# Kernel optimization log

Measured on AMD Instinct MI355X. Metric: run time of the kernel, lower is better.

Reference implementation:

```python
import jax, jax.numpy as jnp
import numpy as np

G = 131072            # number of graphs
NPG = 38              # nodes per graph (from reshape to (*, 38))
N = G * NPG           # total nodes
E = 10 * N            # total edges (avg degree 10)


def leaky_relu(x):
    return jnp.where(x >= 0, x, 0.01 * x)


def setup_inputs() -> dict:
    key = jax.random.key(0)
    ks = jax.random.split(key, 13)
    s = 0.1
    return {
        "x": jax.random.normal(ks[0], (N, 1), jnp.float32),
        "edge_index": jax.random.randint(ks[1], (2, E), 0, N, dtype=jnp.int64)
            if jax.config.read("jax_enable_x64") else jax.random.randint(ks[1], (2, E), 0, N, dtype=jnp.int32),
        "edge_attr": jax.random.normal(ks[2], (E, 1), jnp.float32),
        # NNConv(1,1, Linear(1,1)) params
        "w_edge": jax.random.normal(ks[3], (1, 1), jnp.float32) * s,  # edge MLP weight
        "b_edge": jax.random.normal(ks[4], (1,), jnp.float32) * s,   # edge MLP bias
        "w_root": jax.random.normal(ks[5], (1, 1), jnp.float32) * s, # NNConv root weight
        "b_conv": jax.random.normal(ks[6], (1,), jnp.float32) * s,   # NNConv bias
        # head MLP: 38 -> 4 -> 4 -> 12 (stored as (in, out))
        "W1": jax.random.normal(ks[7], (38, 4), jnp.float32) * s,
        "b1": jax.random.normal(ks[8], (4,), jnp.float32) * s,
        "W2": jax.random.normal(ks[9], (4, 4), jnp.float32) * s,
        "b2": jax.random.normal(ks[10], (4,), jnp.float32) * s,
        "W3": jax.random.normal(ks[11], (4, 12), jnp.float32) * s,
        "b3": jax.random.normal(ks[12], (12,), jnp.float32) * s,
    }


def reference(x, edge_index, edge_attr, w_edge, b_edge, w_root, b_conv,
              W1, b1, W2, b2, W3, b3):
    src, dst = edge_index[0], edge_index[1]
    # per-edge 1x1 transform produced by edge MLP: theta_e = Linear(edge_attr)
    theta = edge_attr @ w_edge + b_edge            # [E, 1]
    # message = x_src * theta (in=out=1 so the matmul is a scalar product)
    msg = x[src] * theta                           # [E, 1] gather + multiply
    agg = jax.ops.segment_sum(msg, dst, num_segments=N)  # scatter-add to targets
    nodes = agg + x @ w_root + b_conv              # [N, 1] add aggr + root + bias
    # dense head over per-graph node vectors (dropout is identity at eval)
    h = nodes.reshape(G, NPG)                      # [G, 38]
    h = leaky_relu(h @ W1 + b1)                    # [G, 4]
    h = leaky_relu(h @ W2 + b2)                    # [G, 4]
    h = leaky_relu(h @ W3 + b3)                    # [G, 12]
    return jax.nn.softmax(h, axis=-1)
```

## Files before the change

kernel.cpp:

```cpp
#include <hip/hip_runtime.h>
#include <hip/hip_fp16.h>

#define NPG 38
#define HEAD_BLK 256
#define SHIFT 13
#define SLICE (1 << SHIFT)
#define DBMAX 640
#define NSB 8
#define NB1 1024
#define P1_THR 512
#define CH 8192
#define P2_THR 512
#define BB_THR 1024
#define BB_PH 1024

typedef int      v4i __attribute__((ext_vector_type(4)));
typedef float    v4f __attribute__((ext_vector_type(4)));
typedef unsigned v2u __attribute__((ext_vector_type(2)));

static inline __device__ unsigned short f2h(float f) {
    return __half_as_ushort(__float2half(f));
}
static inline __device__ float h2f(unsigned short b) {
    return __half2float(__ushort_as_half(b));
}

__global__ __launch_bounds__(P1_THR) void k_p1a(
    const int* __restrict__ src, int nquads, int qpb, int sbsz,
    int* __restrict__ histM8)
{
    __shared__ int h8[NSB];
    const int tid = threadIdx.x;
    if (tid < NSB) h8[tid] = 0;
    __syncthreads();
    const int blk = blockIdx.x;
    const int q0 = blk * qpb;
    const int q1 = min(q0 + qpb, nquads);
    const v4i* s4 = (const v4i*)src;
    for (int q = q0 + tid; q < q1; q += P1_THR) {
        v4i s = __builtin_nontemporal_load(s4 + q);
        atomicAdd(&h8[s.x / sbsz], 1);
        atomicAdd(&h8[s.y / sbsz], 1);
        atomicAdd(&h8[s.z / sbsz], 1);
        atomicAdd(&h8[s.w / sbsz], 1);
    }
    __syncthreads();
    if (tid < NSB) histM8[tid * NB1 + blk] = h8[tid];
}

__global__ __launch_bounds__(512) void k_scanM(
    int* __restrict__ histM8, int* __restrict__ sseg)
{
    __shared__ int stot[NSB];
    __shared__ int sbase[NSB + 1];
    const int tid = threadIdx.x;
    const int wid = tid >> 6, lane = tid & 63;

    const int base = wid * NB1 + lane * (NB1 / 64);
    int vals[NB1 / 64];
    int s = 0;
    #pragma unroll
    for (int k = 0; k < NB1 / 64; ++k) { vals[k] = s; s += histM8[base + k]; }
    int excl = s;
    #pragma unroll
    for (int d = 1; d < 64; d <<= 1) {
        int t = __shfl_up(excl, d, 64);
        if (lane >= d) excl += t;
    }
    excl -= s;
    if (lane == 63) stot[wid] = excl + s;
    __syncthreads();
    if (tid == 0) {
        int run = 0;
        for (int i = 0; i < NSB; ++i) { sbase[i] = run; run += stot[i]; }
        sbase[NSB] = run;
    }
    __syncthreads();
    const int b0 = sbase[wid] + excl;
    #pragma unroll
    for (int k = 0; k < NB1 / 64; ++k) histM8[base + k] = vals[k] + b0;
    if (tid < NSB + 1) sseg[tid] = sbase[tid];
}

__global__ __launch_bounds__(P1_THR) void k_p1b(
    const int* __restrict__ src, const int* __restrict__ dst,
    const float* __restrict__ ea,
    const float* __restrict__ w_edge, const float* __restrict__ b_edge,
    int nquads, int qpb, int sbsz,
    const int* __restrict__ histM8,
    v2u* __restrict__ recs)
{
    __shared__ int cur8[NSB];
    const int blk = blockIdx.x;
    if (threadIdx.x < NSB) cur8[threadIdx.x] = histM8[threadIdx.x * NB1 + blk];
    __syncthreads();
    const int q0 = blk * qpb;
    const int q1 = min(q0 + qpb, nquads);
    const float we = w_edge[0], be = b_edge[0];
    const v4i* s4 = (const v4i*)src;
    const v4i* d4 = (const v4i*)dst;
    const v4f* e4 = (const v4f*)ea;
    for (int q = q0 + threadIdx.x; q < q1; q += P1_THR) {
        v4i s = __builtin_nontemporal_load(s4 + q);
        v4i d = __builtin_nontemporal_load(d4 + q);
        v4f e = __builtin_nontemporal_load(e4 + q);
        #pragma unroll
        for (int k = 0; k < 4; ++k) {
            int sv = (k == 0) ? s.x : (k == 1) ? s.y : (k == 2) ? s.z : s.w;
            int dv = (k == 0) ? d.x : (k == 1) ? d.y : (k == 2) ? d.z : d.w;
            float ev = (k == 0) ? e.x : (k == 1) ? e.y : (k == 2) ? e.z : e.w;
            int sb = sv / sbsz;
            int sl = sv - sb * sbsz;
            unsigned short tb = f2h(fmaf(ev, we, be));
            int p = atomicAdd(&cur8[sb], 1);
            v2u r;
            r.x = ((unsigned)(sl & 0xFFFF) << 16) | (unsigned)tb;
            r.y = (unsigned)dv | ((unsigned)(sl >> 16) << 23);
            recs[p] = r;
        }
    }
}

__global__ __launch_bounds__(P2_THR) void k_p2(
    const v2u* __restrict__ recs, const float* __restrict__ x,
    const int* __restrict__ sseg, int sbsz, int DB, int NCH, int bpx, int E,
    unsigned short* __restrict__ ofsT, unsigned* __restrict__ pairs)
{
    __shared__ __align__(16) unsigned pairbuf[CH];
    __shared__ int hD[DBMAX];
    __shared__ int lofs[DBMAX];
    __shared__ int lcur[DBMAX];
    __shared__ int sS[NSB + 1];

    const int jraw = blockIdx.x;
    const int j = (jraw & 7) * bpx + (jraw >> 3);
    if (j >= NCH) return;
    const int start = j * CH;
    const int n = min(CH, E - start);
    const int tid = threadIdx.x;
    const int wid = tid >> 6, lane = tid & 63;

    if (tid < NSB + 1) sS[tid] = sseg[tid];
    for (int i = tid; i < DBMAX; i += P2_THR) hD[i] = 0;
    __syncthreads();

    #pragma unroll
    for (int half = 0; half < CH / (8 * P2_THR); ++half) {
        unsigned bk[8];
        #pragma unroll
        for (int k = 0; k < 8; ++k) {
            int idx = tid + (half * 8 + k) * P2_THR;
            bk[k] = (idx < n) ? ((recs[start + idx].y & 0x7FFFFFu) >> SHIFT)
                              : 0xFFFFu;
        }
        #pragma unroll
        for (int k = 0; k < 8; ++k)
            if (bk[k] != 0xFFFFu) atomicAdd(&hD[bk[k]], 1);
    }
    __syncthreads();

    if (wid == 0) {
        const int base = lane * (DBMAX / 64);
        int vals[DBMAX / 64];
        int s = 0;
        #pragma unroll
        for (int k = 0; k < DBMAX / 64; ++k) { vals[k] = s; s += hD[base + k]; }
        int excl = s;
        #pragma unroll
        for (int d = 1; d < 64; d <<= 1) {
            int t = __shfl_up(excl, d, 64);
            if (lane >= d) excl += t;
        }
        excl -= s;
        #pragma unroll
        for (int k = 0; k < DBMAX / 64; ++k) lofs[base + k] = vals[k] + excl;
    }
    __syncthreads();

    const size_t tbase = (size_t)j * (DBMAX + 1);
    for (int b = tid; b < DB; b += P2_THR) {
        lcur[b] = lofs[b];
        ofsT[tbase + b] = (unsigned short)lofs[b];
    }
    if (tid == 0) ofsT[tbase + DB] = (unsigned short)n;
    __syncthreads();

    #pragma unroll
    for (int half = 0; half < CH / (8 * P2_THR); ++half) {
        v2u r[8];
        #pragma unroll
        for (int k = 0; k < 8; ++k) {
            int idx = tid + (half * 8 + k) * P2_THR;
            if (idx < n) r[k] = recs[start + idx];
            else { r[k].x = 0u; r[k].y = 0u; }
        }
        float xv[8];
        #pragma unroll
        for (int k = 0; k < 8; ++k) {
            int idx = tid + (half * 8 + k) * P2_THR;
            int gp = start + min(idx, n - 1);
            int sbr = 0;
            #pragma unroll
            for (int s = 1; s < NSB; ++s) sbr += (gp >= sS[s]);
            int sl = (int)(r[k].x >> 16) | (int)((r[k].y >> 23) << 16);
            xv[k] = x[(size_t)sbr * sbsz + sl];
        }
        #pragma unroll
        for (int k = 0; k < 8; ++k) {
            int idx = tid + (half * 8 + k) * P2_THR;
            if (idx < n) {
                unsigned d = r[k].y & 0x7FFFFFu;
                float m = xv[k] * h2f((unsigned short)(r[k].x & 0xFFFFu));
                int li = atomicAdd(&lcur[d >> SHIFT], 1);
                pairbuf[li] = ((d & (SLICE - 1)) << 16) | (unsigned)f2h(m);
            }
        }
    }
    __syncthreads();

    const size_t pbase = (size_t)j * CH;
    uint4* out4 = reinterpret_cast<uint4*>(pairs + pbase);
    const uint4* pb4 = reinterpret_cast<const uint4*>(pairbuf);
    #pragma unroll
    for (int i = 0; i < CH / 4 / P2_THR; ++i)
        out4[tid + i * P2_THR] = pb4[tid + i * P2_THR];
}

__global__ __launch_bounds__(BB_THR) void k_binB(
    const unsigned* __restrict__ pairs,
    const unsigned short* __restrict__ ofsT,
    int NCH, int DB,
    const float* __restrict__ x,
    const float* __restrict__ w_root, const float* __restrict__ b_conv,
    float* __restrict__ nodes, int N)
{
    __shared__ float slice[SLICE];
    __shared__ unsigned short so0[BB_PH];
    __shared__ int spre[BB_PH];
    __shared__ int sTot;
    const int b = blockIdx.x;
    const int tid = threadIdx.x;
    const int wid = tid >> 6, lane = tid & 63;

    for (int i = tid; i < SLICE; i += BB_THR) slice[i] = 0.0f;
    __syncthreads();

    for (int ch0 = 0; ch0 < NCH; ch0 += BB_PH) {
        const int nc = min(BB_PH, NCH - ch0);
        for (int c = tid; c < nc; c += BB_THR) {
            const size_t tb = (size_t)(ch0 + c) * (DBMAX + 1);
            int o0 = ofsT[tb + b];
            int o1 = ofsT[tb + b + 1];
            so0[c] = (unsigned short)o0;
            spre[c] = o1 - o0;
        }
        __syncthreads();
        if (wid == 0) {
            const int base = lane * (BB_PH / 64);
            int vals[BB_PH / 64];
            int s = 0;
            #pragma unroll
            for (int k = 0; k < BB_PH / 64; ++k) {
                int idx = base + k;
                int t = (idx < nc) ? spre[idx] : 0;
                vals[k] = s; s += t;
            }
            int excl = s;
            #pragma unroll
            for (int d = 1; d < 64; d <<= 1) {
                int t = __shfl_up(excl, d, 64);
                if (lane >= d) excl += t;
            }
            excl -= s;
            #pragma unroll
            for (int k = 0; k < BB_PH / 64; ++k) {
                int idx = base + k;
                if (idx < nc) spre[idx] = vals[k] + excl;
            }
            if (lane == 63) sTot = excl + s;
        }
        __syncthreads();
        const int total = sTot;
        for (int i = tid; i < total; i += BB_THR) {
            int lo = 0, hi = nc - 1;
            while (lo < hi) {
                int mid = (lo + hi + 1) >> 1;
                if (spre[mid] <= i) lo = mid; else hi = mid - 1;
            }
            int off = i - spre[lo];
            unsigned p = pairs[(size_t)(ch0 + lo) * CH + so0[lo] + off];
            atomicAdd(&slice[p >> 16], h2f((unsigned short)(p & 0xFFFFu)));
        }
        __syncthreads();
    }

    const float wr = w_root[0], bc = b_conv[0];
    const int gbase = b << SHIFT;
    for (int i = tid; i < SLICE; i += BB_THR) {
        int gi = gbase + i;
        if (gi < N) nodes[gi] = slice[i] + fmaf(__builtin_nontemporal_load(x + gi), wr, bc);
    }
}

__global__ __launch_bounds__(512) void k_count_mid(
    const int* __restrict__ dst, int nquads, int qpb, int DB,
    int* __restrict__ gcntD)
{
    __shared__ int hD[DBMAX];
    for (int i = threadIdx.x; i < DB; i += 512) hD[i] = 0;
    __syncthreads();
    const int q0 = blockIdx.x * qpb;
    const int q1 = min(q0 + qpb, nquads);
    const v4i* d4 = (const v4i*)dst;
    for (int q = q0 + threadIdx.x; q < q1; q += 512) {
        v4i d = __builtin_nontemporal_load(d4 + q);
        atomicAdd(&hD[d.x >> SHIFT], 1);
        atomicAdd(&hD[d.y >> SHIFT], 1);
        atomicAdd(&hD[d.z >> SHIFT], 1);
        atomicAdd(&hD[d.w >> SHIFT], 1);
    }
    __syncthreads();
    for (int i = threadIdx.x; i < DB; i += 512)
        if (hD[i]) atomicAdd(&gcntD[i], hD[i]);
}

__global__ void k_scanD(const int* __restrict__ gcntD, int DB,
                        int* __restrict__ bbaseD, int* __restrict__ gcurD)
{
    if (threadIdx.x == 0 && blockIdx.x == 0) {
        int run = 0;
        for (int i = 0; i < DB; ++i) { bbaseD[i] = run; gcurD[i] = run; run += gcntD[i]; }
        bbaseD[DB] = run;
    }
}

__global__ __launch_bounds__(512) void k_binA_resv(
    const float* __restrict__ x,
    const int* __restrict__ src, const int* __restrict__ dst,
    const float* __restrict__ ea,
    const float* __restrict__ w_edge, const float* __restrict__ b_edge,
    int nquads, int qpb, int DB,
    int* __restrict__ gcurD, unsigned* __restrict__ pairs)
{
    __shared__ int hD[DBMAX];
    __shared__ int cur[DBMAX];
    const int q0 = blockIdx.x * qpb;
    const int q1 = min(q0 + qpb, nquads);
    for (int i = threadIdx.x; i < DB; i += 512) hD[i] = 0;
    __syncthreads();
    const v4i* s4 = (const v4i*)src;
    const v4i* d4 = (const v4i*)dst;
    const v4f* e4 = (const v4f*)ea;
    for (int q = q0 + threadIdx.x; q < q1; q += 512) {
        v4i d = d4[q];
        atomicAdd(&hD[d.x >> SHIFT], 1);
        atomicAdd(&hD[d.y >> SHIFT], 1);
        atomicAdd(&hD[d.z >> SHIFT], 1);
        atomicAdd(&hD[d.w >> SHIFT], 1);
    }
    __syncthreads();
    for (int i = threadIdx.x; i < DB; i += 512) {
        int cnt = hD[i];
        cur[i] = cnt ? atomicAdd(&gcurD[i], cnt) : 0;
    }
    __syncthreads();
    const float we = w_edge[0], be = b_edge[0];
    for (int q = q0 + threadIdx.x; q < q1; q += 512) {
        v4i s = __builtin_nontemporal_load(s4 + q);
        v4i d = d4[q];
        v4f e = __builtin_nontemporal_load(e4 + q);
        #pragma unroll
        for (int k = 0; k < 4; ++k) {
            int sv = (k == 0) ? s.x : (k == 1) ? s.y : (k == 2) ? s.z : s.w;
            unsigned dv = (unsigned)((k == 0) ? d.x : (k == 1) ? d.y : (k == 2) ? d.z : d.w);
            float ev = (k == 0) ? e.x : (k == 1) ? e.y : (k == 2) ? e.z : e.w;
            float m = x[sv] * fmaf(ev, we, be);
            int p = atomicAdd(&cur[dv >> SHIFT], 1);
            pairs[p] = ((dv & (SLICE - 1)) << 16) | (unsigned)f2h(m);
        }
    }
}

__global__ __launch_bounds__(1024) void k_binB_lin(
    const unsigned* __restrict__ pairs,
    const int* __restrict__ bbaseD,
    const float* __restrict__ x,
    const float* __restrict__ w_root, const float* __restrict__ b_conv,
    float* __restrict__ nodes, int N)
{
    __shared__ float slice[SLICE];
    const int b = blockIdx.x;
    for (int i = threadIdx.x; i < SLICE; i += 1024) slice[i] = 0.0f;
    __syncthreads();
    const int p0 = bbaseD[b];
    const int p1 = bbaseD[b + 1];
    for (int i = p0 + threadIdx.x; i < p1; i += 1024) {
        unsigned p = __builtin_nontemporal_load(pairs + i);
        atomicAdd(&slice[p >> 16], h2f((unsigned short)(p & 0xFFFFu)));
    }
    __syncthreads();
    const float wr = w_root[0], bc = b_conv[0];
    const int gbase = b << SHIFT;
    for (int i = threadIdx.x; i < SLICE; i += 1024) {
        int gi = gbase + i;
        if (gi < N) nodes[gi] = slice[i] + fmaf(__builtin_nontemporal_load(x + gi), wr, bc);
    }
}

__global__ __launch_bounds__(256) void edge_kernel_atomic(
    const float* __restrict__ x,
    const int*   __restrict__ src, const int* __restrict__ dst,
    const float* __restrict__ ea,
    const float* __restrict__ w_edge, const float* __restrict__ b_edge,
    float* __restrict__ agg, int E)
{
    const float we = w_edge[0], be = b_edge[0];
    int tid = blockIdx.x * blockDim.x + threadIdx.x;
    int stride = gridDim.x * blockDim.x;
    for (int i = tid; i < E; i += stride)
        atomicAdd(&agg[dst[i]], x[src[i]] * fmaf(ea[i], we, be));
}

__global__ __launch_bounds__(256) void finalize_nodes(
    const float* __restrict__ x, const float* __restrict__ agg,
    const float* __restrict__ w_root, const float* __restrict__ b_conv,
    float* __restrict__ nodes, int N)
{
    const float wr = w_root[0], bc = b_conv[0];
    int i = blockIdx.x * blockDim.x + threadIdx.x;
    int stride = gridDim.x * blockDim.x;
    for (; i < N; i += stride) nodes[i] = agg[i] + fmaf(x[i], wr, bc);
}

__global__ __launch_bounds__(HEAD_BLK) void head_kernel(
    const float* __restrict__ nodes,
    const float* __restrict__ W1, const float* __restrict__ b1,
    const float* __restrict__ W2, const float* __restrict__ b2,
    const float* __restrict__ W3, const float* __restrict__ b3,
    float* __restrict__ out, int G)
{
    __shared__ float s_nodes[HEAD_BLK * NPG];
    __shared__ float s_W1[NPG * 4];
    __shared__ float s_W2[4 * 4];
    __shared__ float s_W3[4 * 12];
    __shared__ float s_b1[4];
    __shared__ float s_b2[4];
    __shared__ float s_b3[12];

    const int tid = threadIdx.x;
    if (tid < NPG * 4) s_W1[tid] = W1[tid];
    if (tid >= 160 && tid < 176) s_W2[tid - 160] = W2[tid - 160];
    if (tid >= 176 && tid < 224) s_W3[tid - 176] = W3[tid - 176];
    if (tid >= 224 && tid < 228) s_b1[tid - 224] = b1[tid - 224];
    if (tid >= 228 && tid < 232) s_b2[tid - 228] = b2[tid - 228];
    if (tid >= 232 && tid < 244) s_b3[tid - 232] = b3[tid - 232];

    const int g0 = blockIdx.x * HEAD_BLK;
    const size_t ebase = (size_t)g0 * NPG;
    const int nelem = HEAD_BLK * NPG;
    const int avail = min(nelem, (G - g0) * NPG);
    for (int i = tid; i < avail; i += HEAD_BLK) s_nodes[i] = nodes[ebase + i];
    __syncthreads();

    const int g = g0 + tid;
    if (g >= G) return;
    const float* nd = &s_nodes[tid * NPG];

    float h1[4];
    #pragma unroll
    for (int k = 0; k < 4; ++k) h1[k] = s_b1[k];
    #pragma unroll
    for (int j = 0; j < NPG; ++j) {
        const float nj = nd[j];
        #pragma unroll
        for (int k = 0; k < 4; ++k) h1[k] = fmaf(nj, s_W1[j * 4 + k], h1[k]);
    }
    #pragma unroll
    for (int k = 0; k < 4; ++k) h1[k] = h1[k] >= 0.0f ? h1[k] : 0.01f * h1[k];

    float h2[4];
    #pragma unroll
    for (int k = 0; k < 4; ++k) {
        float a = s_b2[k];
        #pragma unroll
        for (int j = 0; j < 4; ++j) a = fmaf(h1[j], s_W2[j * 4 + k], a);
        h2[k] = a >= 0.0f ? a : 0.01f * a;
    }

    float h3[12];
    #pragma unroll
    for (int k = 0; k < 12; ++k) {
        float a = s_b3[k];
        #pragma unroll
        for (int j = 0; j < 4; ++j) a = fmaf(h2[j], s_W3[j * 12 + k], a);
        h3[k] = a >= 0.0f ? a : 0.01f * a;
    }

    float m = h3[0];
    #pragma unroll
    for (int k = 1; k < 12; ++k) m = fmaxf(m, h3[k]);
    float sum = 0.0f;
    #pragma unroll
    for (int k = 0; k < 12; ++k) { h3[k] = expf(h3[k] - m); sum += h3[k]; }
    const float inv = 1.0f / sum;

    float4* o = reinterpret_cast<float4*>(out + (size_t)g * 12);
    o[0] = make_float4(h3[0] * inv, h3[1] * inv, h3[2]  * inv, h3[3]  * inv);
    o[1] = make_float4(h3[4] * inv, h3[5] * inv, h3[6]  * inv, h3[7]  * inv);
    o[2] = make_float4(h3[8] * inv, h3[9] * inv, h3[10] * inv, h3[11] * inv);
}

extern "C" void kernel_launch(void* const* d_in, const int* in_sizes, int n_in,
                              void* d_out, int out_size, void* d_ws, size_t ws_size,
                              hipStream_t stream)
{
    const float* x      = (const float*)d_in[0];
    const int*   eidx   = (const int*)  d_in[1];
    const float* ea     = (const float*)d_in[2];
    const float* w_edge = (const float*)d_in[3];
    const float* b_edge = (const float*)d_in[4];
    const float* w_root = (const float*)d_in[5];
    const float* b_conv = (const float*)d_in[6];
    const float* W1 = (const float*)d_in[7];
    const float* b1 = (const float*)d_in[8];
    const float* W2 = (const float*)d_in[9];
    const float* b2 = (const float*)d_in[10];
    const float* W3 = (const float*)d_in[11];
    const float* b3 = (const float*)d_in[12];
    float* out = (float*)d_out;

    const int N = in_sizes[0];
    const int E = in_sizes[2];
    const int G = N / NPG;
    const int* src = eidx;
    const int* dst = eidx + E;
    const int nquads = E / 4;
    const int DB = (N + SLICE - 1) >> SHIFT;

    const int hblocks = (G + HEAD_BLK - 1) / HEAD_BLK;
    char* ws = (char*)d_ws;

    const bool quadok = (E % 4) == 0 && DB <= DBMAX && DB >= 1;
    const int  sbsz   = (N % NSB == 0) ? (N / NSB) : 0;

    const int NCH = (E + CH - 1) / CH;
    const int bpx = (NCH + 7) / 8;

    const size_t META_INTS = (size_t)NSB * NB1 + (NSB + 1) + DBMAX + DBMAX + (DBMAX + 1);

    size_t off_pairs = (size_t)E * 8;
    size_t sz_pairs  = (size_t)NCH * CH * 4;
    size_t off_ofsT  = off_pairs + sz_pairs;
    size_t sz_ofsT   = ((size_t)NCH * (DBMAX + 1) * 2 + 15) & ~(size_t)15;
    size_t off_nodes = off_ofsT + sz_ofsT;
    size_t off_meta  = off_nodes + (size_t)N * 4;
    size_t need_v5   = off_meta + META_INTS * 4;

    size_t off_nodes_mid = (size_t)E * 4;
    size_t off_meta_mid  = off_nodes_mid + (size_t)N * 4;
    size_t need_mid      = off_meta_mid + META_INTS * 4;

    if (quadok && sbsz > 0 && need_v5 <= ws_size) {
        v2u*            recs  = (v2u*)ws;
        unsigned*       pairs = (unsigned*)(ws + off_pairs);
        unsigned short* ofsT  = (unsigned short*)(ws + off_ofsT);
        float*          nodes = (float*)(ws + off_nodes);
        int*            meta  = (int*)(ws + off_meta);
        int* histM8 = meta;
        int* sseg   = meta + NSB * NB1;

        const int qpb = (nquads + NB1 - 1) / NB1;
        k_p1a<<<NB1, P1_THR, 0, stream>>>(src, nquads, qpb, sbsz, histM8);
        k_scanM<<<1, 512, 0, stream>>>(histM8, sseg);
        k_p1b<<<NB1, P1_THR, 0, stream>>>(src, dst, ea, w_edge, b_edge,
                                          nquads, qpb, sbsz, histM8, recs);
        k_p2<<<8 * bpx, P2_THR, 0, stream>>>(recs, x, sseg, sbsz, DB, NCH, bpx,
                                             E, ofsT, pairs);
        k_binB<<<DB, BB_THR, 0, stream>>>(pairs, ofsT, NCH, DB, x,
                                          w_root, b_conv, nodes, N);
        head_kernel<<<hblocks, HEAD_BLK, 0, stream>>>(nodes, W1, b1, W2, b2,
                                                      W3, b3, out, G);
    } else if (quadok && need_mid <= ws_size) {
        unsigned* pairs = (unsigned*)ws;
        float*    nodes = (float*)(ws + off_nodes_mid);
        int*      meta  = (int*)(ws + off_meta_mid);
        int* gcntD  = meta + NSB * NB1 + (NSB + 1);
        int* gcurD  = gcntD + DBMAX;
        int* bbaseD = gcurD + DBMAX;

        hipMemsetAsync(gcntD, 0, DBMAX * sizeof(int), stream);
        const int NBm = 2048;
        const int qpbm = (nquads + NBm - 1) / NBm;
        k_count_mid<<<NBm, 512, 0, stream>>>(dst, nquads, qpbm, DB, gcntD);
        k_scanD<<<1, 64, 0, stream>>>(gcntD, DB, bbaseD, gcurD);
        k_binA_resv<<<NBm, 512, 0, stream>>>(x, src, dst, ea, w_edge, b_edge,
                                             nquads, qpbm, DB, gcurD, pairs);
        k_binB_lin<<<DB, 1024, 0, stream>>>(pairs, bbaseD, x, w_root, b_conv,
                                            nodes, N);
        head_kernel<<<hblocks, HEAD_BLK, 0, stream>>>(nodes, W1, b1, W2, b2,
                                                      W3, b3, out, G);
    } else {
        float* agg   = (float*)d_ws;
        float* nodes = agg + N;
        hipMemsetAsync(agg, 0, (size_t)N * sizeof(float), stream);
        edge_kernel_atomic<<<2048, 256, 0, stream>>>(x, src, dst, ea, w_edge,
                                                     b_edge, agg, E);
        finalize_nodes<<<2048, 256, 0, stream>>>(x, agg, w_root, b_conv, nodes, N);
        head_kernel<<<hblocks, HEAD_BLK, 0, stream>>>(nodes, W1, b1, W2, b2,
                                                      W3, b3, out, G);
    }
}
```

Before: 1.099 ms.

## Replace prefix-scan plus binary search in binB with per-wave chunk-segment processing

The bin-B scatter kernel previously ran a single-wave prefix scan over chunk segment lengths, then had every thread binary-search the prefix array to find its pair. Now each wave takes 8 chunk segments at a time and lanes index directly into each segment, batching 8 loads before issuing the LDS atomics. This removes the serial scan, one barrier and the per-element binary search. In exchange, lanes sit idle whenever a segment is shorter than 64 entries, which is likely given roughly 8192/640 pairs per chunk-bin.

```diff
diff --git a/kernel.cpp b/kernel.cpp
--- a/kernel.cpp
+++ b/kernel.cpp
@@ -12,6 +12,7 @@
 #define CH 8192
 #define P2_THR 512
 #define BB_THR 1024
+#define BB_NW (BB_THR / 64)
 #define BB_PH 1024
 
 typedef int      v4i __attribute__((ext_vector_type(4)));
@@ -236,8 +237,7 @@
 {
     __shared__ float slice[SLICE];
     __shared__ unsigned short so0[BB_PH];
-    __shared__ int spre[BB_PH];
-    __shared__ int sTot;
+    __shared__ unsigned short sln[BB_PH];
     const int b = blockIdx.x;
     const int tid = threadIdx.x;
     const int wid = tid >> 6, lane = tid & 63;
@@ -252,44 +252,38 @@
             int o0 = ofsT[tb + b];
             int o1 = ofsT[tb + b + 1];
             so0[c] = (unsigned short)o0;
-            spre[c] = o1 - o0;
+            sln[c] = (unsigned short)(o1 - o0);
         }
         __syncthreads();
-        if (wid == 0) {
-            const int base = lane * (BB_PH / 64);
-            int vals[BB_PH / 64];
-            int s = 0;
+        for (int c0 = wid * 8; c0 < nc; c0 += BB_NW * 8) {
+            int o0r[8], lnr[8];
             #pragma unroll
-            for (int k = 0; k < BB_PH / 64; ++k) {
-                int idx = base + k;
-                int t = (idx < nc) ? spre[idx] : 0;
-                vals[k] = s; s += t;
+            for (int k = 0; k < 8; ++k) {
+                int c = c0 + k;
+                bool v = c < nc;
+                o0r[k] = v ? (int)so0[c] : 0;
+                lnr[k] = v ? (int)sln[c] : 0;
             }
-            int excl = s;
+            unsigned pr[8];
             #pragma unroll
-            for (int d = 1; d < 64; d <<= 1) {
-                int t = __shfl_up(excl, d, 64);
-                if (lane >= d) excl += t;
+            for (int k = 0; k < 8; ++k) {
+                if (lane < lnr[k])
+                    pr[k] = pairs[(size_t)(ch0 + c0 + k) * CH + o0r[k] + lane];
             }
-            excl -= s;
             #pragma unroll
-            for (int k = 0; k < BB_PH / 64; ++k) {
-                int idx = base + k;
-                if (idx < nc) spre[idx] = vals[k] + excl;
+            for (int k = 0; k < 8; ++k) {
+                if (lane < lnr[k])
+                    atomicAdd(&slice[pr[k] >> 16],
+                              h2f((unsigned short)(pr[k] & 0xFFFFu)));
             }
-            if (lane == 63) sTot = excl + s;
-        }
-        __syncthreads();
-        const int total = sTot;
-        for (int i = tid; i < total; i += BB_THR) {
-            int lo = 0, hi = nc - 1;
-            while (lo < hi) {
-                int mid = (lo + hi + 1) >> 1;
-                if (spre[mid] <= i) lo = mid; else hi = mid - 1;
+            #pragma unroll
+            for (int k = 0; k < 8; ++k) {
+                for (int j2 = lane + 64; j2 < lnr[k]; j2 += 64) {
+                    unsigned p = pairs[(size_t)(ch0 + c0 + k) * CH + o0r[k] + j2];
+                    atomicAdd(&slice[p >> 16],
+                              h2f((unsigned short)(p & 0xFFFFu)));
+                }
             }
-            int off = i - spre[lo];
-            unsigned p = pairs[(size_t)(ch0 + lo) * CH + so0[lo] + off];
-            atomicAdd(&slice[p >> 16], h2f((unsigned short)(p & 0xFFFFu)));
         }
         __syncthreads();
     }
```

Result: no change. 1.108 ms (+0.8%).

## Compact per-chunk bin segments into contiguous buffer before slice accumulation

Applied to the files above, without the earlier changes.

Replaces the binB kernel, which scanned chunk offsets per phase and binary-searched to gather scattered pair segments, with a three-step compaction. The new steps compute per-group bin counts, prefix-sum them, and copy each bin's segments into a contiguous pairs2 buffer (aliasing the recs region). The linear binB kernel then streams contiguous pairs into shared-memory atomics. This removes the per-element binary search and strided gathers, at the cost of an extra full read/write pass over pairs and three more launches, one of them a single-block serial scan.

```diff
diff --git a/kernel.cpp b/kernel.cpp
--- a/kernel.cpp
+++ b/kernel.cpp
@@ -11,8 +11,7 @@
 #define P1_THR 512
 #define CH 8192
 #define P2_THR 512
-#define BB_THR 1024
-#define BB_PH 1024
+#define CGS 64
 
 typedef int      v4i __attribute__((ext_vector_type(4)));
 typedef float    v4f __attribute__((ext_vector_type(4)));
@@ -226,77 +225,143 @@
         out4[tid + i * P2_THR] = pb4[tid + i * P2_THR];
 }
 
-__global__ __launch_bounds__(BB_THR) void k_binB(
+__global__ __launch_bounds__(1024) void k_sum1(
+    const unsigned short* __restrict__ ofsT,
+    int NCH, int DB, int* __restrict__ partial)
+{
+    const int cg = blockIdx.x;
+    const int j0 = cg * CGS;
+    const int jn = min(CGS, NCH - j0);
+    const int b = threadIdx.x;
+    if (b >= DB) return;
+    int acc = 0;
+    for (int k = 0; k < jn; ++k) {
+        size_t tb = (size_t)(j0 + k) * (DBMAX + 1);
+        acc += (int)ofsT[tb + b + 1] - (int)ofsT[tb + b];
+    }
+    partial[(size_t)cg * DB + b] = acc;
+}
+
+__global__ __launch_bounds__(1024) void k_sum2(
+    const int* __restrict__ partial, int ncg, int DB,
+    int* __restrict__ groupbase, int* __restrict__ bbaseD)
+{
+    __shared__ int btot[DBMAX];
+    __shared__ int bofs[DBMAX];
+    const int tid = threadIdx.x;
+    const int wid = tid >> 6, lane = tid & 63;
+    for (int i = tid; i < DBMAX; i += 1024) btot[i] = 0;
+    __syncthreads();
+    if (tid < DB) {
+        int run = 0;
+        for (int cg = 0; cg < ncg; ++cg) {
+            int t = partial[(size_t)cg * DB + tid];
+            groupbase[(size_t)cg * DB + tid] = run;
+            run += t;
+        }
+        btot[tid] = run;
+    }
+    __syncthreads();
+    if (wid == 0) {
+        const int base = lane * (DBMAX / 64);
+        int vals[DBMAX / 64];
+        int s = 0;
+        #pragma unroll
+        for (int k = 0; k < DBMAX / 64; ++k) { vals[k] = s; s += btot[base + k]; }
+        int excl = s;
+        #pragma unroll
+        for (int d = 1; d < 64; d <<= 1) {
+            int t = __shfl_up(excl, d, 64);
+            if (lane >= d) excl += t;
+        }
+        excl -= s;
+        #pragma unroll
+        for (int k = 0; k < DBMAX / 64; ++k) bofs[base + k] = vals[k] + excl;
+    }
+    __syncthreads();
+    if (tid < DB) {
+        int bb = bofs[tid];
+        bbaseD[tid] = bb;
+        for (int cg = 0; cg < ncg; ++cg)
+            groupbase[(size_t)cg * DB + tid] += bb;
+    }
+    if (tid == DB - 1) bbaseD[DB] = bofs[tid] + btot[tid];
+}
+
+__global__ __launch_bounds__(1024) void k_p2b(
     const unsigned* __restrict__ pairs,
     const unsigned short* __restrict__ ofsT,
-    int NCH, int DB,
+    const int* __restrict__ groupbase,
+    int NCH, int DB, int ncg,
+    unsigned* __restrict__ pairs2)
+{
+    const int g  = blockIdx.x & 7;
+    const int cg = blockIdx.x >> 3;
+    if (cg >= ncg) return;
+    const int bpb = (DB + 7) >> 3;
+    const int b0 = g * bpb;
+    const int b1 = min(b0 + bpb, DB);
+    const int j0 = cg * CGS;
+    const int jn = min(CGS, NCH - j0);
+    const int wid = threadIdx.x >> 6, lane = threadIdx.x & 63;
+
+    for (int b = b0 + wid; b < b1; b += 16) {
+        int cur = groupbase[(size_t)cg * DB + b];
+        int o0 = 0, len = 0;
+        if (lane < jn) {
+            size_t tb = (size_t)(j0 + lane) * (DBMAX + 1);
+            o0 = ofsT[tb + b];
+            len = (int)ofsT[tb + b + 1] - o0;
+        }
+        for (int k = 0; k < jn; k += 8) {
+            int ro[8], rl[8], rc[8];
+            int c = cur;
+            #pragma unroll
+            for (int u = 0; u < 8; ++u) {
+                int l = __shfl(len, k + u, 64);
+                ro[u] = __shfl(o0, k + u, 64);
+                rl[u] = (k + u < jn) ? l : 0;
+                rc[u] = c; c += rl[u];
+            }
+            unsigned v[8];
+            #pragma unroll
+            for (int u = 0; u < 8; ++u)
+                if (lane < rl[u])
+                    v[u] = pairs[(size_t)(j0 + k + u) * CH + ro[u] + lane];
+            #pragma unroll
+            for (int u = 0; u < 8; ++u)
+                if (lane < rl[u]) pairs2[rc[u] + lane] = v[u];
+            #pragma unroll
+            for (int u = 0; u < 8; ++u)
+                for (int t = lane + 64; t < rl[u]; t += 64)
+                    pairs2[rc[u] + t] =
+                        pairs[(size_t)(j0 + k + u) * CH + ro[u] + t];
+            cur = c;
+        }
+    }
+}
+
+__global__ __launch_bounds__(1024) void k_binB_lin(
+    const unsigned* __restrict__ pairs,
+    const int* __restrict__ bbaseD,
     const float* __restrict__ x,
     const float* __restrict__ w_root, const float* __restrict__ b_conv,
     float* __restrict__ nodes, int N)
 {
     __shared__ float slice[SLICE];
-    __shared__ unsigned short so0[BB_PH];
-    __shared__ int spre[BB_PH];
-    __shared__ int sTot;
     const int b = blockIdx.x;
-    const int tid = threadIdx.x;
-    const int wid = tid >> 6, lane = tid & 63;
-
-    for (int i = tid; i < SLICE; i += BB_THR) slice[i] = 0.0f;
-    __syncthreads();
-
-    for (int ch0 = 0; ch0 < NCH; ch0 += BB_PH) {
-        const int nc = min(BB_PH, NCH - ch0);
-        for (int c = tid; c < nc; c += BB_THR) {
-            const size_t tb = (size_t)(ch0 + c) * (DBMAX + 1);
-            int o0 = ofsT[tb + b];
-            int o1 = ofsT[tb + b + 1];
-            so0[c] = (unsigned short)o0;
-            spre[c] = o1 - o0;
-        }
-        __syncthreads();
-        if (wid == 0) {
-            const int base = lane * (BB_PH / 64);
-            int vals[BB_PH / 64];
-            int s = 0;
-            #pragma unroll
-            for (int k = 0; k < BB_PH / 64; ++k) {
-                int idx = base + k;
-                int t = (idx < nc) ? spre[idx] : 0;
-                vals[k] = s; s += t;
-            }
-            int excl = s;
-            #pragma unroll
-            for (int d = 1; d < 64; d <<= 1) {
-                int t = __shfl_up(excl, d, 64);
-                if (lane >= d) excl += t;
-            }
-            excl -= s;
-            #pragma unroll
-            for (int k = 0; k < BB_PH / 64; ++k) {
-                int idx = base + k;
-                if (idx < nc) spre[idx] = vals[k] + excl;
-            }
-            if (lane == 63) sTot = excl + s;
-        }
-        __syncthreads();
-        const int total = sTot;
-        for (int i = tid; i < total; i += BB_THR) {
-            int lo = 0, hi = nc - 1;
-            while (lo < hi) {
-                int mid = (lo + hi + 1) >> 1;
-                if (spre[mid] <= i) lo = mid; else hi = mid - 1;
-            }
-            int off = i - spre[lo];
-            unsigned p = pairs[(size_t)(ch0 + lo) * CH + so0[lo] + off];
-            atomicAdd(&slice[p >> 16], h2f((unsigned short)(p & 0xFFFFu)));
-        }
-        __syncthreads();
-    }
-
+    for (int i = threadIdx.x; i < SLICE; i += 1024) slice[i] = 0.0f;
+    __syncthreads();
+    const int p0 = bbaseD[b];
+    const int p1 = bbaseD[b + 1];
+    for (int i = p0 + threadIdx.x; i < p1; i += 1024) {
+        unsigned p = __builtin_nontemporal_load(pairs + i);
+        atomicAdd(&slice[p >> 16], h2f((unsigned short)(p & 0xFFFFu)));
+    }
+    __syncthreads();
     const float wr = w_root[0], bc = b_conv[0];
     const int gbase = b << SHIFT;
-    for (int i = tid; i < SLICE; i += BB_THR) {
+    for (int i = threadIdx.x; i < SLICE; i += 1024) {
         int gi = gbase + i;
         if (gi < N) nodes[gi] = slice[i] + fmaf(__builtin_nontemporal_load(x + gi), wr, bc);
     }
@@ -378,32 +443,6 @@
             int p = atomicAdd(&cur[dv >> SHIFT], 1);
             pairs[p] = ((dv & (SLICE - 1)) << 16) | (unsigned)f2h(m);
         }
-    }
-}
-
-__global__ __launch_bounds__(1024) void k_binB_lin(
-    const unsigned* __restrict__ pairs,
-    const int* __restrict__ bbaseD,
-    const float* __restrict__ x,
-    const float* __restrict__ w_root, const float* __restrict__ b_conv,
-    float* __restrict__ nodes, int N)
-{
-    __shared__ float slice[SLICE];
-    const int b = blockIdx.x;
-    for (int i = threadIdx.x; i < SLICE; i += 1024) slice[i] = 0.0f;
-    __syncthreads();
-    const int p0 = bbaseD[b];
-    const int p1 = bbaseD[b + 1];
-    for (int i = p0 + threadIdx.x; i < p1; i += 1024) {
-        unsigned p = __builtin_nontemporal_load(pairs + i);
-        atomicAdd(&slice[p >> 16], h2f((unsigned short)(p & 0xFFFFu)));
-    }
-    __syncthreads();
-    const float wr = w_root[0], bc = b_conv[0];
-    const int gbase = b << SHIFT;
-    for (int i = threadIdx.x; i < SLICE; i += 1024) {
-        int gi = gbase + i;
-        if (gi < N) nodes[gi] = slice[i] + fmaf(__builtin_nontemporal_load(x + gi), wr, bc);
     }
 }
 
@@ -545,8 +584,10 @@
 
     const int NCH = (E + CH - 1) / CH;
     const int bpx = (NCH + 7) / 8;
-
-    const size_t META_INTS = (size_t)NSB * NB1 + (NSB + 1) + DBMAX + DBMAX + (DBMAX + 1);
+    const int ncg = (NCH + CGS - 1) / CGS;
+
+    const size_t META_INTS = (size_t)NSB * NB1 + (NSB + 1) + DBMAX + DBMAX
+                           + (DBMAX + 1) + 2 * (size_t)ncg * DBMAX;
 
     size_t off_pairs = (size_t)E * 8;
     size_t sz_pairs  = (size_t)NCH * CH * 4;
@@ -554,20 +595,24 @@
     size_t sz_ofsT   = ((size_t)NCH * (DBMAX + 1) * 2 + 15) & ~(size_t)15;
     size_t off_nodes = off_ofsT + sz_ofsT;
     size_t off_meta  = off_nodes + (size_t)N * 4;
-    size_t need_v5   = off_meta + META_INTS * 4;
+    size_t need_v6   = off_meta + META_INTS * 4;
 
     size_t off_nodes_mid = (size_t)E * 4;
     size_t off_meta_mid  = off_nodes_mid + (size_t)N * 4;
     size_t need_mid      = off_meta_mid + META_INTS * 4;
 
-    if (quadok && sbsz > 0 && need_v5 <= ws_size) {
-        v2u*            recs  = (v2u*)ws;
-        unsigned*       pairs = (unsigned*)(ws + off_pairs);
-        unsigned short* ofsT  = (unsigned short*)(ws + off_ofsT);
-        float*          nodes = (float*)(ws + off_nodes);
-        int*            meta  = (int*)(ws + off_meta);
-        int* histM8 = meta;
-        int* sseg   = meta + NSB * NB1;
+    if (quadok && sbsz > 0 && need_v6 <= ws_size) {
+        v2u*            recs   = (v2u*)ws;
+        unsigned*       pairs2 = (unsigned*)ws;
+        unsigned*       pairs  = (unsigned*)(ws + off_pairs);
+        unsigned short* ofsT   = (unsigned short*)(ws + off_ofsT);
+        float*          nodes  = (float*)(ws + off_nodes);
+        int*            meta   = (int*)(ws + off_meta);
+        int* histM8    = meta;
+        int* sseg      = histM8 + NSB * NB1;
+        int* bbaseD    = sseg + (NSB + 1) + DBMAX + DBMAX;
+        int* partial   = bbaseD + (DBMAX + 1);
+        int* groupbase = partial + (size_t)ncg * DBMAX;
 
         const int qpb = (nquads + NB1 - 1) / NB1;
         k_p1a<<<NB1, P1_THR, 0, stream>>>(src, nquads, qpb, sbsz, histM8);
@@ -576,8 +621,12 @@
                                           nquads, qpb, sbsz, histM8, recs);
         k_p2<<<8 * bpx, P2_THR, 0, stream>>>(recs, x, sseg, sbsz, DB, NCH, bpx,
                                              E, ofsT, pairs);
-        k_binB<<<DB, BB_THR, 0, stream>>>(pairs, ofsT, NCH, DB, x,
-                                          w_root, b_conv, nodes, N);
+        k_sum1<<<ncg, 1024, 0, stream>>>(ofsT, NCH, DB, partial);
+        k_sum2<<<1, 1024, 0, stream>>>(partial, ncg, DB, groupbase, bbaseD);
+        k_p2b<<<8 * ncg, 1024, 0, stream>>>(pairs, ofsT, groupbase, NCH, DB,
+                                            ncg, pairs2);
+        k_binB_lin<<<DB, 1024, 0, stream>>>(pairs2, bbaseD, x, w_root, b_conv,
+                                            nodes, N);
         head_kernel<<<hblocks, HEAD_BLK, 0, stream>>>(nodes, W1, b1, W2, b2,
                                                       W3, b3, out, G);
     } else if (quadok && need_mid <= ws_size) {
```

Result: slower. 1.217 ms (+10.7%).
